# Performance work log

Hardware: AMD Instinct MI355X
Metric: run time of the kernel (lower is better)

The kernel has to match this reference:

```python
import jax, jax.numpy as jnp
import numpy as np

B, LINS, LHIS, LACT = 128, 64, 128, 32
VOCAB, ACTSZ = 2000, 100
INS_H, INS_E = 256, 128
ACT_E, ACT_IN, ACT_H = 128, 512, 512
POS_E, COL_E, COL_H = 32, 32, 32
ENV = 7 * (POS_E + COL_H)  # 448


def _lstm_cell(h, c, x, Wih, Whh, bih, bhh):
    # torch LSTM gate order: i, f, g, o
    g = x @ Wih.T + h @ Whh.T + bih + bhh
    i, f, gg, o = jnp.split(g, 4, axis=-1)
    c = jax.nn.sigmoid(f) * c + jax.nn.sigmoid(i) * jnp.tanh(gg)
    h = jax.nn.sigmoid(o) * jnp.tanh(c)
    return h, c


def _run_lstm(xs, Wih, Whh, bih, bhh):
    # xs: [T, N, D] -> hs: [T, N, H], zero initial state (torch default)
    N = xs.shape[1]
    H = Whh.shape[1]
    h0 = jnp.zeros((N, H), xs.dtype)

    def step(carry, x):
        h, c = carry
        h, c = _lstm_cell(h, c, x, Wih, Whh, bih, bhh)
        return (h, c), h

    _, hs = jax.lax.scan(step, (h0, h0), xs)
    return hs


def _bilstm_encode(tokens, emb, Wf, Uf, bf1, bf2, Wb, Ub, bb1, bb2):
    xs = emb[tokens].transpose(1, 0, 2)            # [L, B, E]
    hf = _run_lstm(xs, Wf, Uf, bf1, bf2)           # [L, B, H]
    hb = _run_lstm(xs[::-1], Wb, Ub, bb1, bb2)[::-1]
    return jnp.concatenate([hf, hb], -1).transpose(1, 0, 2)  # [B, L, 2H]


def _env_encode(tokens, color_emb, pos_emb, Wih, Whh, bih, bhh):
    # tokens: [B, 35] = 7 beakers x (id + 4 color slots)
    t = tokens.reshape(B, 7, 5)
    col = color_emb[t[:, :, 1:5]]                  # [B, 7, 4, COL_E]
    xs = col.reshape(B * 7, 4, COL_E).transpose(1, 0, 2)  # [4, B*7, COL_E]
    h_last = _run_lstm(xs, Wih, Whh, bih, bhh)[-1].reshape(B, 7, COL_H)
    pos = jnp.broadcast_to(pos_emb[None], (B, 7, POS_E))
    return jnp.concatenate([pos, h_last], -1).reshape(B, 7 * (POS_E + COL_H))


def _attend(A, H, q):
    # Faithful to attend(): scores = sum_k (H @ W)[b,l,k] * q[b,k]; softmax over l;
    # A = H @ W is query-independent so it is hoisted out of the decode loop.
    a = jax.nn.softmax(jnp.einsum('blk,bk->bl', A, q), axis=1)
    return jnp.einsum('bl,bld->bd', a, H)


def _forward(ins_tokens, his_tokens, actions, cur_env, ini_env,
             enc_emb, enc_Wih_f, enc_Whh_f, enc_bih_f, enc_bhh_f,
             enc_Wih_b, enc_Whh_b, enc_bih_b, enc_bhh_b,
             color_emb, pos_emb, ws_Wih, ws_Whh, ws_bih, ws_bhh,
             act_emb, W_c, W_p, W_sb1, W_sb2, W_sc1, W_sc2,
             Wbd_W, Wbd_b, dec_Wih, dec_Whh, dec_bih, dec_bhh,
             h2a_W, h2a_b, h0, c0):
    ins_enc = _bilstm_encode(ins_tokens, enc_emb, enc_Wih_f, enc_Whh_f, enc_bih_f,
                             enc_bhh_f, enc_Wih_b, enc_Whh_b, enc_bih_b, enc_bhh_b)
    his_enc = _bilstm_encode(his_tokens, enc_emb, enc_Wih_f, enc_Whh_f, enc_bih_f,
                             enc_bhh_f, enc_Wih_b, enc_Whh_b, enc_bih_b, enc_bhh_b)
    cur_ctx = _env_encode(cur_env, color_emb, pos_emb, ws_Wih, ws_Whh, ws_bih, ws_bhh)
    ini_ctx = _env_encode(ini_env, color_emb, pos_emb, ws_Wih, ws_Whh, ws_bih, ws_bhh)

    X = act_emb[actions]                            # [B, T, ACT_E]
    # Query-independent projections, hoisted out of the per-step loop (same math).
    A_c = jnp.einsum('bld,dk->blk', ins_enc, W_c)   # [B, LINS, ACT_H]
    A_p = jnp.einsum('bld,dk->blk', his_enc, W_p)   # [B, LHIS, ACT_H+2*INS_H]
    K = ACT_H + 2 * INS_H
    ini_rep = jnp.broadcast_to(ini_ctx[:, None, :], (B, LACT, ENV))
    cur_rep = jnp.broadcast_to(cur_ctx[:, None, :], (B, LACT, ENV))
    A_b1 = jnp.broadcast_to((ini_ctx @ W_sb1)[:, None, :], (B, LACT, K))
    A_b2 = jnp.broadcast_to((ini_ctx @ W_sb2)[:, None, :], (B, LACT, K))
    A_c1 = jnp.broadcast_to((cur_ctx @ W_sc1)[:, None, :], (B, LACT, K))
    A_c2 = jnp.broadcast_to((cur_ctx @ W_sc2)[:, None, :], (B, LACT, K))

    def step(carry, x_t):
        h, c = carry
        z_c = _attend(A_c, ins_enc, h)              # [B, 2*INS_H]
        q = jnp.concatenate([h, z_c], -1)           # [B, ACT_H+2*INS_H]
        z_p = _attend(A_p, his_enc, q)
        z_s1 = jnp.concatenate([_attend(A_b1, ini_rep, q),
                                _attend(A_b2, ini_rep, q)], -1)
        z_sk = jnp.concatenate([_attend(A_c1, cur_rep, q),
                                _attend(A_c2, cur_rep, q)], -1)
        hk1 = jnp.concatenate([z_c, z_p, z_s1, z_sk, x_t], -1)  # [B, 2944]
        hk = jnp.tanh(hk1 @ Wbd_W.T + Wbd_b)        # [B, ACT_IN]
        h, c = _lstm_cell(h, c, hk, dec_Wih, dec_Whh, dec_bih, dec_bhh)
        return (h, c), h

    _, outs = jax.lax.scan(step, (h0, c0), X.transpose(1, 0, 2))
    logits = outs.transpose(1, 0, 2) @ h2a_W.T + h2a_b  # [B, LACT, ACTSZ]
    return logits


def setup_inputs() -> dict:
    root = jax.random.key(0)
    ki = iter(jax.random.split(root, 40))

    def nrm(shape, s=0.05):
        return jax.random.normal(next(ki), shape, dtype=jnp.float32) * s

    inp = {}
    inp['ins_tokens'] = jax.random.randint(next(ki), (B, LINS), 0, VOCAB)
    inp['his_tokens'] = jax.random.randint(next(ki), (B, LHIS), 0, VOCAB)
    inp['actions'] = jax.random.randint(next(ki), (B, LACT), 0, ACTSZ)
    inp['cur_env'] = jax.random.randint(next(ki), (B, 35), 0, 7)
    inp['ini_env'] = jax.random.randint(next(ki), (B, 35), 0, 7)
    inp['enc_emb'] = nrm((VOCAB, INS_E))
    inp['enc_Wih_f'] = nrm((4 * INS_H, INS_E))
    inp['enc_Whh_f'] = nrm((4 * INS_H, INS_H))
    inp['enc_bih_f'] = nrm((4 * INS_H,))
    inp['enc_bhh_f'] = nrm((4 * INS_H,))
    inp['enc_Wih_b'] = nrm((4 * INS_H, INS_E))
    inp['enc_Whh_b'] = nrm((4 * INS_H, INS_H))
    inp['enc_bih_b'] = nrm((4 * INS_H,))
    inp['enc_bhh_b'] = nrm((4 * INS_H,))
    inp['color_emb'] = nrm((7, COL_E))
    inp['pos_emb'] = nrm((7, POS_E))
    inp['ws_Wih'] = nrm((4 * COL_H, COL_E))
    inp['ws_Whh'] = nrm((4 * COL_H, COL_H))
    inp['ws_bih'] = nrm((4 * COL_H,))
    inp['ws_bhh'] = nrm((4 * COL_H,))
    inp['act_emb'] = nrm((ACTSZ, ACT_E))
    inp['W_c'] = nrm((2 * INS_H, ACT_H))
    inp['W_p'] = nrm((2 * INS_H, 2 * INS_H + ACT_H))
    inp['W_sb1'] = nrm((ENV, ACT_H + 2 * INS_H))
    inp['W_sb2'] = nrm((ENV, ACT_H + 2 * INS_H))
    inp['W_sc1'] = nrm((ENV, ACT_H + 2 * INS_H))
    inp['W_sc2'] = nrm((ENV, ACT_H + 2 * INS_H))
    inp['Wbd_W'] = nrm((ACT_IN, 4 * ENV + 4 * INS_H + ACT_E))
    inp['Wbd_b'] = nrm((ACT_IN,))
    inp['dec_Wih'] = nrm((4 * ACT_H, ACT_IN))
    inp['dec_Whh'] = nrm((4 * ACT_H, ACT_H))
    inp['dec_bih'] = nrm((4 * ACT_H,))
    inp['dec_bhh'] = nrm((4 * ACT_H,))
    inp['h2a_W'] = nrm((ACTSZ, ACT_H))
    inp['h2a_b'] = nrm((ACTSZ,))
    inp['h0'] = nrm((B, ACT_H))
    inp['c0'] = nrm((B, ACT_H))
    return inp


def reference(ins_tokens, his_tokens, actions, cur_env, ini_env,
              enc_emb, enc_Wih_f, enc_Whh_f, enc_bih_f, enc_bhh_f,
              enc_Wih_b, enc_Whh_b, enc_bih_b, enc_bhh_b,
              color_emb, pos_emb, ws_Wih, ws_Whh, ws_bih, ws_bhh,
              act_emb, W_c, W_p, W_sb1, W_sb2, W_sc1, W_sc2,
              Wbd_W, Wbd_b, dec_Wih, dec_Whh, dec_bih, dec_bhh,
              h2a_W, h2a_b, h0, c0):
    return _forward(ins_tokens, his_tokens, actions, cur_env, ini_env,
                    enc_emb, enc_Wih_f, enc_Whh_f, enc_bih_f, enc_bhh_f,
                    enc_Wih_b, enc_Whh_b, enc_bih_b, enc_bhh_b,
                    color_emb, pos_emb, ws_Wih, ws_Whh, ws_bih, ws_bhh,
                    act_emb, W_c, W_p, W_sb1, W_sb2, W_sc1, W_sc2,
                    Wbd_W, Wbd_b, dec_Wih, dec_Whh, dec_bih, dec_bhh,
                    h2a_W, h2a_b, h0, c0)
```

## Files before the change

kernel.cpp:

```cpp
#include <hip/hip_runtime.h>


typedef unsigned short u16;
typedef __attribute__((ext_vector_type(8))) short bf16x8;
typedef __attribute__((ext_vector_type(4))) float f32x4;

#define DEVFN static __device__ __forceinline__

DEVFN float bf2f(u16 u) {
  unsigned int x = ((unsigned int)u) << 16;
  float f; __builtin_memcpy(&f, &x, 4); return f;
}
DEVFN u16 f2bf(float f) {
  unsigned int x; __builtin_memcpy(&x, &f, 4);
  x = (x + 0x7fffu + ((x >> 16) & 1u)) >> 16;
  return (u16)x;
}
DEVFN float sigf(float x) { return 1.f / (1.f + __expf(-x)); }
DEVFN bf16x8 load8(const u16* p) { return *(const bf16x8*)p; }
DEVFN int clampi(int v, int lo, int hi) { return v < lo ? lo : (v > hi ? hi : v); }

struct GemmArgs {
  const u16* A; int lda; int M;
  const u16* W; int ldw; int N; int K;
  void* out; int ldc;
  const float* bias;
  const float* hk_base; const float* proj_act; const int* actions; int t;
};

template <int EPI>
__global__ __launch_bounds__(256) void gemm_k(GemmArgs g) {
  int lane = threadIdx.x & 63;
  int wave = threadIdx.x >> 6;
  int col = lane & 15, q = lane >> 4;
  int m0 = blockIdx.x * 64 + (wave >> 1) * 32;
  int n0 = blockIdx.y * 64 + (wave & 1) * 32;
  f32x4 acc[2][2] = {};
  int rA[2] = { m0 + col, m0 + 16 + col };
  int rB[2] = { n0 + col, n0 + 16 + col };
  bool gA[2] = { rA[0] < g.M, rA[1] < g.M };
  bool gB[2] = { rB[0] < g.N, rB[1] < g.N };
  const u16* pA[2]; const u16* pB[2];
#pragma unroll
  for (int i = 0; i < 2; i++) {
    pA[i] = g.A + (size_t)(gA[i] ? rA[i] : 0) * g.lda + q * 8;
    pB[i] = g.W + (size_t)(gB[i] ? rB[i] : 0) * g.ldw + q * 8;
  }
  bf16x8 zf = {0,0,0,0,0,0,0,0};
  for (int k = 0; k < g.K; k += 32) {
    bf16x8 a0 = gA[0] ? load8(pA[0] + k) : zf;
    bf16x8 a1 = gA[1] ? load8(pA[1] + k) : zf;
    bf16x8 b0 = gB[0] ? load8(pB[0] + k) : zf;
    bf16x8 b1 = gB[1] ? load8(pB[1] + k) : zf;
    acc[0][0] = __builtin_amdgcn_mfma_f32_16x16x32_bf16(a0, b0, acc[0][0], 0, 0, 0);
    acc[0][1] = __builtin_amdgcn_mfma_f32_16x16x32_bf16(a0, b1, acc[0][1], 0, 0, 0);
    acc[1][0] = __builtin_amdgcn_mfma_f32_16x16x32_bf16(a1, b0, acc[1][0], 0, 0, 0);
    acc[1][1] = __builtin_amdgcn_mfma_f32_16x16x32_bf16(a1, b1, acc[1][1], 0, 0, 0);
  }
#pragma unroll
  for (int mi = 0; mi < 2; mi++)
#pragma unroll
    for (int ni = 0; ni < 2; ni++)
#pragma unroll
      for (int r = 0; r < 4; r++) {
        int m = m0 + mi * 16 + q * 4 + r;
        int n = n0 + ni * 16 + col;
        if (m >= g.M || n >= g.N) continue;
        float v = acc[mi][ni][r];
        if constexpr (EPI == 0) {
          if (g.bias) v += g.bias[n];
          ((float*)g.out)[(size_t)m * g.ldc + n] = v;
        } else {
          ((u16*)g.out)[(size_t)m * g.ldc + n] = f2bf(v);
        }
      }
}

template <int EPI>
__global__ __launch_bounds__(256) void gemm32_k(GemmArgs g) {
  int lane = threadIdx.x & 63;
  int wave = threadIdx.x >> 6;
  int col = lane & 15, q = lane >> 4;
  int m0 = blockIdx.x * 32 + (wave >> 1) * 16;
  int n0 = blockIdx.y * 32 + (wave & 1) * 16;
  f32x4 acc = {};
  int rA = m0 + col, rB = n0 + col;
  bool gA = rA < g.M, gB = rB < g.N;
  const u16* pA = g.A + (size_t)(gA ? rA : 0) * g.lda + q * 8;
  const u16* pB = g.W + (size_t)(gB ? rB : 0) * g.ldw + q * 8;
  bf16x8 zf = {0,0,0,0,0,0,0,0};
  for (int k = 0; k < g.K; k += 32) {
    bf16x8 a = gA ? load8(pA + k) : zf;
    bf16x8 b = gB ? load8(pB + k) : zf;
    acc = __builtin_amdgcn_mfma_f32_16x16x32_bf16(a, b, acc, 0, 0, 0);
  }
#pragma unroll
  for (int r = 0; r < 4; r++) {
    int m = m0 + q * 4 + r;
    int n = n0 + col;
    if (m >= g.M || n >= g.N) continue;
    float v = acc[r];
    if constexpr (EPI == 0) {
      if (g.bias) v += g.bias[n];
      ((float*)g.out)[(size_t)m * g.ldc + n] = v;
    } else {
      int act = clampi(g.actions[m * 32 + g.t], 0, 99);
      v += g.hk_base[m * 512 + n] + g.proj_act[(size_t)act * 512 + n];
      ((u16*)g.out)[(size_t)m * g.ldc + n] = f2bf(tanhf(v));
    }
  }
}

__global__ __launch_bounds__(256) void dec_gates_cell32(
    const u16* zin_cur, const u16* Wih, const u16* Whh, const float* bias_int,
    float* c_ws, u16* zin_nxt, u16* qbuf, u16* outs, int t) {
  int lane = threadIdx.x & 63, wave = threadIdx.x >> 6;
  int col = lane & 15, q = lane >> 4;
  int m0 = blockIdx.x * 32 + (wave >> 1) * 16;
  int n0 = blockIdx.y * 32 + (wave & 1) * 16;
  f32x4 acc = {};
  const u16* pA = zin_cur + (size_t)(m0 + col) * 1024 + q * 8;
  int r = n0 + col;
  int src = (r & 3) * 512 + (r >> 2);
  const u16* pI = Wih + (size_t)src * 512 + q * 8;
  const u16* pH = Whh + (size_t)src * 512 + q * 8;
  for (int k = 0; k < 512; k += 32) {
    acc = __builtin_amdgcn_mfma_f32_16x16x32_bf16(load8(pA + k), load8(pI + k), acc, 0, 0, 0);
  }
  for (int k = 0; k < 512; k += 32) {
    acc = __builtin_amdgcn_mfma_f32_16x16x32_bf16(load8(pA + 512 + k), load8(pH + k), acc, 0, 0, 0);
  }
  __shared__ float ls[32][36];
#pragma unroll
  for (int rr = 0; rr < 4; rr++) {
    int ml = (wave >> 1) * 16 + q * 4 + rr;
    int nl = (wave & 1) * 16 + col;
    ls[ml][nl] = acc[rr] + bias_int[blockIdx.y * 32 + nl];
  }
  __syncthreads();
  int m = threadIdx.x & 31, jloc = threadIdx.x >> 5;
  int gm = blockIdx.x * 32 + m;
  int j = blockIdx.y * 8 + jloc;
  float gi = ls[m][jloc * 4 + 0];
  float gf = ls[m][jloc * 4 + 1];
  float gg = ls[m][jloc * 4 + 2];
  float go = ls[m][jloc * 4 + 3];
  float cn = sigf(gf) * c_ws[gm * 512 + j] + sigf(gi) * tanhf(gg);
  c_ws[gm * 512 + j] = cn;
  float hn = sigf(go) * tanhf(cn);
  u16 hb = f2bf(hn);
  zin_nxt[(size_t)gm * 1024 + 512 + j] = hb;
  qbuf[(size_t)gm * 1024 + j] = hb;
  outs[((size_t)gm * 32 + t) * 512 + j] = hb;
}

struct CvtJob { const float* src; u16* dst; int R; int C; int ld; int c0; int tr; int blk0; };
struct CvtJobs { CvtJob j[15]; int njobs; };

__global__ void cvt_all(CvtJobs a) {
  int bid = blockIdx.x;
  int ji = 0;
  while (ji + 1 < a.njobs && bid >= a.j[ji + 1].blk0) ji++;
  CvtJob jb = a.j[ji];
  int idx = (bid - jb.blk0) * 256 + threadIdx.x;
  int n = jb.R * jb.C;
  if (idx >= n) return;
  int r = idx / jb.C, c = idx - r * jb.C;
  float v = jb.src[(size_t)r * jb.ld + jb.c0 + c];
  if (jb.tr) jb.dst[(size_t)c * jb.R + r] = f2bf(v);
  else jb.dst[idx] = f2bf(v);
}

__global__ void prep_small(
    const float* bih_f, const float* bhh_f, float* bias_f,
    const float* bih_b, const float* bhh_b, float* bias_b,
    const float* Wbd_b, float* bwbd,
    const float* h2a_b, float* bh2a,
    const float* dec_bih, const float* dec_bhh, float* bdecint) {
  int i = blockIdx.x * 256 + threadIdx.x;
  if (i < 1024) bias_f[i] = bih_f[i] + bhh_f[i];
  else if (i < 2048) { int k = i - 1024; bias_b[k] = bih_b[k] + bhh_b[k]; }
  else if (i < 2560) { int k = i - 2048; bwbd[k] = Wbd_b[k]; }
  else if (i < 2660) { int k = i - 2560; bh2a[k] = h2a_b[k]; }
  else if (i < 4708) {
    int r = i - 2660;
    int j = r >> 2, gg = r & 3;
    bdecint[r] = dec_bih[gg * 512 + j] + dec_bhh[gg * 512 + j];
  }
}

__global__ void wsum_build(const float* Wbd, u16* Wsum) {
  int idx = blockIdx.x * 256 + threadIdx.x;
  int n = idx / 896, j = idx % 896;
  int c1 = (j < 448) ? (1024 + j) : (1920 + (j - 448));
  int c2 = c1 + 448;
  Wsum[idx] = f2bf(Wbd[(size_t)n * 2944 + c1] + Wbd[(size_t)n * 2944 + c2]);
}

__global__ __launch_bounds__(256) void env_encode(
    const int* cur_env, const int* ini_env,
    const float* color_emb, const float* pos_emb,
    const float* wih, const float* whh, const float* bih, const float* bhh,
    u16* ctx_cat) {
  __shared__ float s_wih[128 * 33], s_whh[128 * 33], s_b[128], s_col[7 * 32];
  __shared__ float h_lds[8][33];
  int tid = threadIdx.x;
  for (int i = tid; i < 128 * 32; i += 256) {
    int r = i >> 5, k2 = i & 31;
    s_wih[r * 33 + k2] = wih[i];
    s_whh[r * 33 + k2] = whh[i];
  }
  for (int i = tid; i < 128; i += 256) s_b[i] = bih[i] + bhh[i];
  for (int i = tid; i < 224; i += 256) s_col[i] = color_emb[i];
  int sl = tid >> 5, j = tid & 31;
  int gseq = blockIdx.x * 8 + sl;
  int e = gseq / 896, rem = gseq % 896;
  int b = rem / 7, p = rem % 7;
  const int* env = e ? ini_env : cur_env;
  int eoff = e ? 0 : 448;
  h_lds[sl][j] = 0.f;
  __syncthreads();
  float cj = 0.f, hj = 0.f;
  for (int st = 0; st < 4; st++) {
    int tok = clampi(env[b * 35 + p * 5 + 1 + st], 0, 6);
    const float* x = &s_col[tok * 32];
    float pi = s_b[j], pf = s_b[32 + j], pg = s_b[64 + j], po = s_b[96 + j];
    for (int k = 0; k < 32; k++) {
      float xk = x[k], hk = h_lds[sl][k];
      pi += s_wih[j * 33 + k] * xk + s_whh[j * 33 + k] * hk;
      pf += s_wih[(32 + j) * 33 + k] * xk + s_whh[(32 + j) * 33 + k] * hk;
      pg += s_wih[(64 + j) * 33 + k] * xk + s_whh[(64 + j) * 33 + k] * hk;
      po += s_wih[(96 + j) * 33 + k] * xk + s_whh[(96 + j) * 33 + k] * hk;
    }
    cj = sigf(pf) * cj + sigf(pi) * tanhf(pg);
    hj = sigf(po) * tanhf(cj);
    __syncthreads();
    h_lds[sl][j] = hj;
    __syncthreads();
  }
  size_t base = (size_t)b * 896 + eoff + p * 64;
  ctx_cat[base + j] = f2bf(pos_emb[p * 32 + j]);
  ctx_cat[base + 32 + j] = f2bf(hj);
}

#define HBUF ((size_t)4 * 128 * 256)
__global__ __launch_bounds__(128) void enc_step3(
    int t, int chainbase,
    const int* ins_tok, const int* his_tok,
    const float* projE_f, const float* projE_b,
    const u16* whh_f, const u16* whh_b,
    const float* bias_f, const float* bias_b,
    u16* h_enc, float* c_enc,
    u16* ins_enc, u16* his_enc) {
  int chain = chainbase + (blockIdx.x >> 6);
  int sub = blockIdx.x & 63;
  int sgrp = sub >> 3, jq = sub & 7;
  int w = threadIdx.x >> 6, lane = threadIdx.x & 63;
  int col = lane & 15, q = lane >> 4;
  int dir = chain & 1, his = chain >> 1;
  int L = his ? 128 : 64;
  const int* toks = his ? his_tok : ins_tok;
  int t_x = dir ? (L - 1 - t) : t;
  const float* projE = dir ? projE_b : projE_f;
  const u16* whh = dir ? whh_b : whh_f;
  const float* bias = dir ? bias_b : bias_f;
  const u16* h_rd = h_enc + ((size_t)((t & 1) ^ 1)) * HBUF + (size_t)chain * 128 * 256;
  u16* h_wr = h_enc + ((size_t)(t & 1)) * HBUF + (size_t)chain * 128 * 256;
  float* c_g = c_enc + (size_t)chain * 128 * 256;
  u16* out = his ? his_enc : ins_enc;

  int jw = jq * 32 + w * 16;
  f32x4 acc[4] = {};
  if (t > 0) {
    const u16* hrow = h_rd + (size_t)(sgrp * 16 + col) * 256 + q * 8;
    const u16* wrow[4];
#pragma unroll
    for (int G = 0; G < 4; G++) wrow[G] = whh + (size_t)(G * 256 + jw + col) * 256 + q * 8;
    for (int k = 0; k < 256; k += 32) {
      bf16x8 a = load8(hrow + k);
#pragma unroll
      for (int G = 0; G < 4; G++) {
        bf16x8 bb = load8(wrow[G] + k);
        acc[G] = __builtin_amdgcn_mfma_f32_16x16x32_bf16(a, bb, acc[G], 0, 0, 0);
      }
    }
  }
  int j = jw + col;
  float bi = bias[j], bf = bias[256 + j], bg = bias[512 + j], bo = bias[768 + j];
#pragma unroll
  for (int r = 0; r < 4; r++) {
    int s = q * 4 + r;
    int b = sgrp * 16 + s;
    int tok = clampi(toks[b * L + t_x], 0, 1999);
    const float* px = projE + (size_t)tok * 1024;
    float pi = acc[0][r] + px[j] + bi;
    float pf = acc[1][r] + px[256 + j] + bf;
    float pg = acc[2][r] + px[512 + j] + bg;
    float po = acc[3][r] + px[768 + j] + bo;
    float cold = (t > 0) ? c_g[b * 256 + j] : 0.f;
    float cn = sigf(pf) * cold + sigf(pi) * tanhf(pg);
    float hn = sigf(po) * tanhf(cn);
    c_g[b * 256 + j] = cn;
    u16 hb = f2bf(hn);
    h_wr[b * 256 + j] = hb;
    out[((size_t)b * L + t_x) * 512 + dir * 256 + j] = hb;
  }
}

__global__ __launch_bounds__(256) void attn1(
    const u16* A_c, const u16* insenc, u16* qattn, u16* qbuf) {
  int b = blockIdx.x, tid = threadIdx.x;
  __shared__ float su[512], red[256], aw[64];
  __shared__ float zacc[4][512];
  for (int d = tid; d < 512; d += 256) su[d] = bf2f(qbuf[(size_t)b * 1024 + d]);
  __syncthreads();
  {
    int l = tid >> 2, part = tid & 3;
    const u16* row = A_c + ((size_t)b * 64 + l) * 512 + part * 128;
    float s = 0.f;
    for (int k = 0; k < 128; k += 8) {
      bf16x8 v = load8(row + k);
#pragma unroll
      for (int e = 0; e < 8; e++) s += bf2f((u16)v[e]) * su[part * 128 + k + e];
    }
    red[tid] = s;
  }
  __syncthreads();
  if (tid < 64) {
    float sc = red[tid * 4] + red[tid * 4 + 1] + red[tid * 4 + 2] + red[tid * 4 + 3];
    float m = sc;
    for (int off = 32; off > 0; off >>= 1) m = fmaxf(m, __shfl_xor(m, off));
    float e = __expf(sc - m);
    float sm = e;
    for (int off = 32; off > 0; off >>= 1) sm += __shfl_xor(sm, off);
    aw[tid] = e / sm;
  }
  __syncthreads();
  {
    int part = tid >> 6, chunk = tid & 63;
    float a[8] = {};
    for (int l = part * 16; l < part * 16 + 16; l++) {
      bf16x8 v = load8(insenc + ((size_t)b * 64 + l) * 512 + chunk * 8);
      float w = aw[l];
#pragma unroll
      for (int e = 0; e < 8; e++) a[e] += w * bf2f((u16)v[e]);
    }
#pragma unroll
    for (int e = 0; e < 8; e++) zacc[part][chunk * 8 + e] = a[e];
  }
  __syncthreads();
  for (int d = tid; d < 512; d += 256) {
    float z = zacc[0][d] + zacc[1][d] + zacc[2][d] + zacc[3][d];
    u16 zb = f2bf(z);
    qattn[(size_t)b * 1024 + d] = zb;
    qbuf[(size_t)b * 1024 + 512 + d] = zb;
  }
}

__global__ __launch_bounds__(256) void attn2(
    const float* u_p, const u16* hisenc, u16* qattn) {
  int b = blockIdx.x, tid = threadIdx.x;
  __shared__ float su[512], red[256], aw[128], mr[2];
  __shared__ float zacc[4][512];
  for (int d = tid; d < 512; d += 256) su[d] = u_p[b * 512 + d];
  __syncthreads();
  {
    int l = tid >> 1, part = tid & 1;
    const u16* row = hisenc + ((size_t)b * 128 + l) * 512 + part * 256;
    float s = 0.f;
    for (int k = 0; k < 256; k += 8) {
      bf16x8 v = load8(row + k);
#pragma unroll
      for (int e = 0; e < 8; e++) s += bf2f((u16)v[e]) * su[part * 256 + k + e];
    }
    red[tid] = s;
  }
  __syncthreads();
  float sc = (tid < 128) ? red[tid * 2] + red[tid * 2 + 1] : 0.f;
  __syncthreads();
  if (tid < 128) red[tid] = sc;
  __syncthreads();
  if (tid < 64) {
    float m = fmaxf(red[tid], red[tid + 64]);
    for (int off = 32; off > 0; off >>= 1) m = fmaxf(m, __shfl_xor(m, off));
    if (tid == 0) mr[0] = m;
  }
  __syncthreads();
  float ex = 0.f;
  if (tid < 128) { ex = __expf(sc - mr[0]); red[tid] = ex; }
  __syncthreads();
  if (tid < 64) {
    float s2 = red[tid] + red[tid + 64];
    for (int off = 32; off > 0; off >>= 1) s2 += __shfl_xor(s2, off);
    if (tid == 0) mr[1] = s2;
  }
  __syncthreads();
  if (tid < 128) aw[tid] = ex / mr[1];
  __syncthreads();
  {
    int part = tid >> 6, chunk = tid & 63;
    float a[8] = {};
    for (int l = part * 32; l < part * 32 + 32; l++) {
      bf16x8 v = load8(hisenc + ((size_t)b * 128 + l) * 512 + chunk * 8);
      float w = aw[l];
#pragma unroll
      for (int e = 0; e < 8; e++) a[e] += w * bf2f((u16)v[e]);
    }
#pragma unroll
    for (int e = 0; e < 8; e++) zacc[part][chunk * 8 + e] = a[e];
  }
  __syncthreads();
  for (int d = tid; d < 512; d += 256) {
    float z = zacc[0][d] + zacc[1][d] + zacc[2][d] + zacc[3][d];
    qattn[(size_t)b * 1024 + 512 + d] = f2bf(z);
  }
}

__global__ void dec_init(const float* h0, const float* c0, u16* zin0, u16* qbuf, float* c_ws) {
  int idx = blockIdx.x * 256 + threadIdx.x;
  int b = idx >> 9, d = idx & 511;
  u16 hv = f2bf(h0[idx]);
  zin0[(size_t)b * 1024 + 512 + d] = hv;
  qbuf[(size_t)b * 1024 + d] = hv;
  c_ws[idx] = c0[idx];
}

extern "C" void kernel_launch(void* const* d_in, const int* in_sizes, int n_in,
                              void* d_out, int out_size, void* d_ws, size_t ws_size,
                              hipStream_t stream) {
  const int* ins_tok = (const int*)d_in[0];
  const int* his_tok = (const int*)d_in[1];
  const int* actions = (const int*)d_in[2];
  const int* cur_env = (const int*)d_in[3];
  const int* ini_env = (const int*)d_in[4];
  const float* enc_emb = (const float*)d_in[5];
  const float* Wih_f = (const float*)d_in[6];
  const float* Whh_f = (const float*)d_in[7];
  const float* bih_f = (const float*)d_in[8];
  const float* bhh_f = (const float*)d_in[9];
  const float* Wih_b = (const float*)d_in[10];
  const float* Whh_b = (const float*)d_in[11];
  const float* bih_b = (const float*)d_in[12];
  const float* bhh_b = (const float*)d_in[13];
  const float* color_emb = (const float*)d_in[14];
  const float* pos_emb = (const float*)d_in[15];
  const float* ws_Wih = (const float*)d_in[16];
  const float* ws_Whh = (const float*)d_in[17];
  const float* ws_bih = (const float*)d_in[18];
  const float* ws_bhh = (const float*)d_in[19];
  const float* act_emb = (const float*)d_in[20];
  const float* W_c = (const float*)d_in[21];
  const float* W_p = (const float*)d_in[22];
  const float* Wbd_W = (const float*)d_in[27];
  const float* Wbd_b = (const float*)d_in[28];
  const float* dec_Wih = (const float*)d_in[29];
  const float* dec_Whh = (const float*)d_in[30];
  const float* dec_bih = (const float*)d_in[31];
  const float* dec_bhh = (const float*)d_in[32];
  const float* h2a_W = (const float*)d_in[33];
  const float* h2a_b = (const float*)d_in[34];
  const float* h0 = (const float*)d_in[35];
  const float* c0 = (const float*)d_in[36];
  (void)in_sizes; (void)n_in; (void)out_size; (void)ws_size;

  char* ws = (char*)d_ws;
  size_t off = 0;
  auto alloc = [&](size_t bytes) -> char* {
    char* p = ws + off;
    off = (off + bytes + 255) & ~(size_t)255;
    return p;
  };
  u16* insenc   = (u16*)alloc(8192ull * 512 * 2);
  u16* hisenc   = (u16*)alloc(16384ull * 512 * 2);
  u16* outs     = (u16*)alloc(4096ull * 512 * 2);
  u16* Wsum     = (u16*)alloc(512ull * 896 * 2);
  u16* h_enc    = (u16*)alloc(2 * HBUF * 2);
  float* c_enc  = (float*)alloc(4ull * 128 * 256 * 4);
  float* projact= (float*)alloc(100ull * 512 * 4);
  float* bias_f = (float*)alloc(1024 * 4);
  float* bias_b = (float*)alloc(1024 * 4);
  float* bdecint= (float*)alloc(2048 * 4);
  float* bwbd   = (float*)alloc(512 * 4);
  float* bh2a   = (float*)alloc(128 * 4);
  u16* ctxcat   = (u16*)alloc(128ull * 896 * 2);
  float* hkbase = (float*)alloc(128ull * 512 * 4);
  float* u_p    = (float*)alloc(128ull * 512 * 4);
  u16* qbuf     = (u16*)alloc(128ull * 1024 * 2);
  u16* qattn    = (u16*)alloc(128ull * 1024 * 2);
  u16* zin      = (u16*)alloc(2ull * 128 * 1024 * 2);
  float* c_dec  = (float*)alloc(128ull * 512 * 4);
  float* projE_f = (float*)alloc(2000ull * 1024 * 4);
  float* projE_b = (float*)alloc(2000ull * 1024 * 4);
  u16* A_c      = (u16*)alloc(8192ull * 512 * 2);
  u16* emb_bf   = (u16*)alloc(2000ull * 128 * 2);
  u16* wihf_bf  = (u16*)alloc(1024ull * 128 * 2);
  u16* wihb_bf  = (u16*)alloc(1024ull * 128 * 2);
  u16* whhf_bf  = (u16*)alloc(1024ull * 256 * 2);
  u16* whhb_bf  = (u16*)alloc(1024ull * 256 * 2);
  u16* act_bf   = (u16*)alloc(100ull * 128 * 2);
  u16* wcT_bf   = (u16*)alloc(512ull * 512 * 2);
  u16* wp_bf    = (u16*)alloc(512ull * 1024 * 2);
  u16* wbd01_bf = (u16*)alloc(512ull * 1024 * 2);
  u16* wbdx_bf  = (u16*)alloc(512ull * 128 * 2);
  u16* dwih_bf  = (u16*)alloc(2048ull * 512 * 2);
  u16* dwhh_bf  = (u16*)alloc(2048ull * 512 * 2);
  u16* h2a_bf   = (u16*)alloc(100ull * 512 * 2);

  CvtJobs cj{};
  int nb = 0, jn = 0;
  auto addjob = [&](const float* s, u16* d, int R, int C, int ld, int c0c, int tr) {
    cj.j[jn] = { s, d, R, C, ld, c0c, tr, nb };
    nb += (R * C + 255) / 256;
    jn++;
  };
  addjob(enc_emb, emb_bf, 2000, 128, 128, 0, 0);
  addjob(Wih_f, wihf_bf, 1024, 128, 128, 0, 0);
  addjob(Wih_b, wihb_bf, 1024, 128, 128, 0, 0);
  addjob(Whh_f, whhf_bf, 1024, 256, 256, 0, 0);
  addjob(Whh_b, whhb_bf, 1024, 256, 256, 0, 0);
  addjob(act_emb, act_bf, 100, 128, 128, 0, 0);
  addjob(W_c, wcT_bf, 512, 512, 512, 0, 1);
  addjob(W_p, wp_bf, 512, 1024, 1024, 0, 0);
  addjob(Wbd_W, wbd01_bf, 512, 1024, 2944, 0, 0);
  addjob(Wbd_W, wbdx_bf, 512, 128, 2944, 2816, 0);
  addjob(dec_Wih, dwih_bf, 2048, 512, 512, 0, 0);
  addjob(dec_Whh, dwhh_bf, 2048, 512, 512, 0, 0);
  addjob(h2a_W, h2a_bf, 100, 512, 512, 0, 0);
  cj.njobs = jn;
  cvt_all<<<nb, 256, 0, stream>>>(cj);

  prep_small<<<19, 256, 0, stream>>>(bih_f, bhh_f, bias_f, bih_b, bhh_b, bias_b,
                                     Wbd_b, bwbd, h2a_b, bh2a,
                                     dec_bih, dec_bhh, bdecint);
  wsum_build<<<1792, 256, 0, stream>>>(Wbd_W, Wsum);

  {
    GemmArgs ge = {};
    ge.A = emb_bf; ge.lda = 128; ge.M = 2000; ge.W = wihf_bf; ge.ldw = 128;
    ge.N = 1024; ge.K = 128; ge.out = projE_f; ge.ldc = 1024;
    gemm_k<0><<<dim3(32, 16), 256, 0, stream>>>(ge);
    ge.W = wihb_bf; ge.out = projE_b;
    gemm_k<0><<<dim3(32, 16), 256, 0, stream>>>(ge);
  }

  GemmArgs gp = {};
  gp.A = act_bf; gp.lda = 128; gp.M = 100; gp.W = wbdx_bf; gp.ldw = 128;
  gp.N = 512; gp.K = 128; gp.out = projact; gp.ldc = 512; gp.bias = bwbd;
  gemm_k<0><<<dim3(2, 8), 256, 0, stream>>>(gp);

  env_encode<<<224, 256, 0, stream>>>(cur_env, ini_env, color_emb, pos_emb,
                                      ws_Wih, ws_Whh, ws_bih, ws_bhh, ctxcat);
  GemmArgs gb = {};
  gb.A = ctxcat; gb.lda = 896; gb.M = 128; gb.W = Wsum; gb.ldw = 896;
  gb.N = 512; gb.K = 896; gb.out = hkbase; gb.ldc = 512;
  gemm_k<0><<<dim3(2, 8), 256, 0, stream>>>(gb);

  for (int t = 0; t < 128; t++) {
    int cb = (t < 64) ? 0 : 2;
    int nbk = (t < 64) ? 256 : 128;
    enc_step3<<<nbk, 128, 0, stream>>>(t, cb, ins_tok, his_tok,
                                       projE_f, projE_b, whhf_bf, whhb_bf,
                                       bias_f, bias_b, h_enc, c_enc,
                                       insenc, hisenc);
  }

  {
    GemmArgs ga = {};
    ga.A = insenc; ga.lda = 512; ga.M = 8192; ga.W = wcT_bf; ga.ldw = 512;
    ga.N = 512; ga.K = 512; ga.out = A_c; ga.ldc = 512;
    gemm_k<1><<<dim3(128, 8), 256, 0, stream>>>(ga);
  }

  dec_init<<<256, 256, 0, stream>>>(h0, c0, zin, qbuf, c_dec);
  for (int t = 0; t < 32; t++) {
    u16* zin_cur = zin + (size_t)(t & 1) * 128 * 1024;
    u16* zin_nxt = zin + (size_t)((t + 1) & 1) * 128 * 1024;
    attn1<<<128, 256, 0, stream>>>(A_c, insenc, qattn, qbuf);
    GemmArgs gv = {};
    gv.A = qbuf; gv.lda = 1024; gv.M = 128; gv.W = wp_bf; gv.ldw = 1024;
    gv.N = 512; gv.K = 1024; gv.out = u_p; gv.ldc = 512;
    gemm32_k<0><<<dim3(4, 16), 256, 0, stream>>>(gv);
    attn2<<<128, 256, 0, stream>>>(u_p, hisenc, qattn);
    GemmArgs gh = {};
    gh.A = qattn; gh.lda = 1024; gh.M = 128; gh.W = wbd01_bf; gh.ldw = 1024;
    gh.N = 512; gh.K = 1024; gh.out = zin_cur; gh.ldc = 1024;
    gh.hk_base = hkbase; gh.proj_act = projact; gh.actions = actions; gh.t = t;
    gemm32_k<2><<<dim3(4, 16), 256, 0, stream>>>(gh);
    dec_gates_cell32<<<dim3(4, 64), 256, 0, stream>>>(
        zin_cur, dwih_bf, dwhh_bf, bdecint, c_dec, zin_nxt, qbuf, outs, t);
  }

  GemmArgs gl = {};
  gl.A = outs; gl.lda = 512; gl.M = 4096; gl.W = h2a_bf; gl.ldw = 512;
  gl.N = 100; gl.K = 512; gl.out = d_out; gl.ldc = 100; gl.bias = bh2a;
  gemm32_k<0><<<dim3(128, 4), 256, 0, stream>>>(gl);
}
```

Measured before the change: 2.716 ms.

## Widen decoder attention blocks, split u_p GEMM over K halves, fold dec_init into prep

Both attention kernels in the decode loop now use 512 threads per block, so each thread covers half as much of the score and context reductions. The W_p projection GEMM is split into two K-halves that write separate partial outputs, doubling the grid; attn2 adds the two partials when it loads its query. The decoder state initialisation moves into prep_small to save one launch. The aim is more parallelism and shorter per-step latency in the 32-step decode loop, at the cost of more shared memory per block and an extra partial buffer.

```diff
diff --git a/kernel.cpp b/kernel.cpp
--- a/kernel.cpp
+++ b/kernel.cpp
@@ -111,6 +111,30 @@
   }
 }
 
+__global__ __launch_bounds__(256) void up_split(
+    const u16* qbuf, const u16* wp, float* u_p2) {
+  int lane = threadIdx.x & 63;
+  int wave = threadIdx.x >> 6;
+  int col = lane & 15, q = lane >> 4;
+  int half = blockIdx.y >> 4;
+  int by = blockIdx.y & 15;
+  int m0 = blockIdx.x * 32 + (wave >> 1) * 16;
+  int n0 = by * 32 + (wave & 1) * 16;
+  f32x4 acc = {};
+  const u16* pA = qbuf + (size_t)(m0 + col) * 1024 + half * 512 + q * 8;
+  const u16* pB = wp + (size_t)(n0 + col) * 1024 + half * 512 + q * 8;
+  for (int k = 0; k < 512; k += 32) {
+    acc = __builtin_amdgcn_mfma_f32_16x16x32_bf16(load8(pA + k), load8(pB + k), acc, 0, 0, 0);
+  }
+  float* out = u_p2 + (size_t)half * 128 * 512;
+#pragma unroll
+  for (int r = 0; r < 4; r++) {
+    int m = m0 + q * 4 + r;
+    int n = n0 + col;
+    out[(size_t)m * 512 + n] = acc[r];
+  }
+}
+
 __global__ __launch_bounds__(256) void dec_gates_cell32(
     const u16* zin_cur, const u16* Wih, const u16* Whh, const float* bias_int,
     float* c_ws, u16* zin_nxt, u16* qbuf, u16* outs, int t) {
@@ -176,7 +200,8 @@
     const float* bih_b, const float* bhh_b, float* bias_b,
     const float* Wbd_b, float* bwbd,
     const float* h2a_b, float* bh2a,
-    const float* dec_bih, const float* dec_bhh, float* bdecint) {
+    const float* dec_bih, const float* dec_bhh, float* bdecint,
+    const float* h0, const float* c0, u16* zin0, u16* qbuf, float* c_ws) {
   int i = blockIdx.x * 256 + threadIdx.x;
   if (i < 1024) bias_f[i] = bih_f[i] + bhh_f[i];
   else if (i < 2048) { int k = i - 1024; bias_b[k] = bih_b[k] + bhh_b[k]; }
@@ -186,6 +211,13 @@
     int r = i - 2660;
     int j = r >> 2, gg = r & 3;
     bdecint[r] = dec_bih[gg * 512 + j] + dec_bhh[gg * 512 + j];
+  } else if (i < 4708 + 128 * 512) {
+    int k = i - 4708;
+    int b = k >> 9, d = k & 511;
+    u16 hv = f2bf(h0[k]);
+    zin0[(size_t)b * 1024 + 512 + d] = hv;
+    qbuf[(size_t)b * 1024 + d] = hv;
+    c_ws[k] = c0[k];
   }
 }
 
@@ -307,27 +339,29 @@
   }
 }
 
-__global__ __launch_bounds__(256) void attn1(
+__global__ __launch_bounds__(512) void attn1(
     const u16* A_c, const u16* insenc, u16* qattn, u16* qbuf) {
   int b = blockIdx.x, tid = threadIdx.x;
-  __shared__ float su[512], red[256], aw[64];
-  __shared__ float zacc[4][512];
-  for (int d = tid; d < 512; d += 256) su[d] = bf2f(qbuf[(size_t)b * 1024 + d]);
-  __syncthreads();
-  {
-    int l = tid >> 2, part = tid & 3;
-    const u16* row = A_c + ((size_t)b * 64 + l) * 512 + part * 128;
+  __shared__ float su[512], red[512], aw[64];
+  __shared__ float zacc[8][512];
+  su[tid] = bf2f(qbuf[(size_t)b * 1024 + tid]);
+  __syncthreads();
+  {
+    int l = tid >> 3, part = tid & 7;
+    const u16* row = A_c + ((size_t)b * 64 + l) * 512 + part * 64;
     float s = 0.f;
-    for (int k = 0; k < 128; k += 8) {
+    for (int k = 0; k < 64; k += 8) {
       bf16x8 v = load8(row + k);
 #pragma unroll
-      for (int e = 0; e < 8; e++) s += bf2f((u16)v[e]) * su[part * 128 + k + e];
+      for (int e = 0; e < 8; e++) s += bf2f((u16)v[e]) * su[part * 64 + k + e];
     }
     red[tid] = s;
   }
   __syncthreads();
   if (tid < 64) {
-    float sc = red[tid * 4] + red[tid * 4 + 1] + red[tid * 4 + 2] + red[tid * 4 + 3];
+    float sc = 0.f;
+#pragma unroll
+    for (int i = 0; i < 8; i++) sc += red[tid * 8 + i];
     float m = sc;
     for (int off = 32; off > 0; off >>= 1) m = fmaxf(m, __shfl_xor(m, off));
     float e = __expf(sc - m);
@@ -339,7 +373,7 @@
   {
     int part = tid >> 6, chunk = tid & 63;
     float a[8] = {};
-    for (int l = part * 16; l < part * 16 + 16; l++) {
+    for (int l = part * 8; l < part * 8 + 8; l++) {
       bf16x8 v = load8(insenc + ((size_t)b * 64 + l) * 512 + chunk * 8);
       float w = aw[l];
 #pragma unroll
@@ -349,34 +383,36 @@
     for (int e = 0; e < 8; e++) zacc[part][chunk * 8 + e] = a[e];
   }
   __syncthreads();
-  for (int d = tid; d < 512; d += 256) {
-    float z = zacc[0][d] + zacc[1][d] + zacc[2][d] + zacc[3][d];
+  {
+    float z = zacc[0][tid] + zacc[1][tid] + zacc[2][tid] + zacc[3][tid]
+            + zacc[4][tid] + zacc[5][tid] + zacc[6][tid] + zacc[7][tid];
     u16 zb = f2bf(z);
-    qattn[(size_t)b * 1024 + d] = zb;
-    qbuf[(size_t)b * 1024 + 512 + d] = zb;
-  }
-}
-
-__global__ __launch_bounds__(256) void attn2(
-    const float* u_p, const u16* hisenc, u16* qattn) {
+    qattn[(size_t)b * 1024 + tid] = zb;
+    qbuf[(size_t)b * 1024 + 512 + tid] = zb;
+  }
+}
+
+__global__ __launch_bounds__(512) void attn2(
+    const float* u_p2, const u16* hisenc, u16* qattn) {
   int b = blockIdx.x, tid = threadIdx.x;
-  __shared__ float su[512], red[256], aw[128], mr[2];
-  __shared__ float zacc[4][512];
-  for (int d = tid; d < 512; d += 256) su[d] = u_p[b * 512 + d];
-  __syncthreads();
-  {
-    int l = tid >> 1, part = tid & 1;
-    const u16* row = hisenc + ((size_t)b * 128 + l) * 512 + part * 256;
+  __shared__ float su[512], red[512], aw[128], mr[2];
+  __shared__ float zacc[8][512];
+  su[tid] = u_p2[(size_t)b * 512 + tid] + u_p2[65536 + (size_t)b * 512 + tid];
+  __syncthreads();
+  {
+    int l = tid >> 2, part = tid & 3;
+    const u16* row = hisenc + ((size_t)b * 128 + l) * 512 + part * 128;
     float s = 0.f;
-    for (int k = 0; k < 256; k += 8) {
+    for (int k = 0; k < 128; k += 8) {
       bf16x8 v = load8(row + k);
 #pragma unroll
-      for (int e = 0; e < 8; e++) s += bf2f((u16)v[e]) * su[part * 256 + k + e];
+      for (int e = 0; e < 8; e++) s += bf2f((u16)v[e]) * su[part * 128 + k + e];
     }
     red[tid] = s;
   }
   __syncthreads();
-  float sc = (tid < 128) ? red[tid * 2] + red[tid * 2 + 1] : 0.f;
+  float sc = 0.f;
+  if (tid < 128) sc = red[tid * 4] + red[tid * 4 + 1] + red[tid * 4 + 2] + red[tid * 4 + 3];
   __syncthreads();
   if (tid < 128) red[tid] = sc;
   __syncthreads();
@@ -400,7 +436,7 @@
   {
     int part = tid >> 6, chunk = tid & 63;
     float a[8] = {};
-    for (int l = part * 32; l < part * 32 + 32; l++) {
+    for (int l = part * 16; l < part * 16 + 16; l++) {
       bf16x8 v = load8(hisenc + ((size_t)b * 128 + l) * 512 + chunk * 8);
       float w = aw[l];
 #pragma unroll
@@ -410,19 +446,11 @@
     for (int e = 0; e < 8; e++) zacc[part][chunk * 8 + e] = a[e];
   }
   __syncthreads();
-  for (int d = tid; d < 512; d += 256) {
-    float z = zacc[0][d] + zacc[1][d] + zacc[2][d] + zacc[3][d];
-    qattn[(size_t)b * 1024 + 512 + d] = f2bf(z);
-  }
-}
-
-__global__ void dec_init(const float* h0, const float* c0, u16* zin0, u16* qbuf, float* c_ws) {
-  int idx = blockIdx.x * 256 + threadIdx.x;
-  int b = idx >> 9, d = idx & 511;
-  u16 hv = f2bf(h0[idx]);
-  zin0[(size_t)b * 1024 + 512 + d] = hv;
-  qbuf[(size_t)b * 1024 + d] = hv;
-  c_ws[idx] = c0[idx];
+  {
+    float z = zacc[0][tid] + zacc[1][tid] + zacc[2][tid] + zacc[3][tid]
+            + zacc[4][tid] + zacc[5][tid] + zacc[6][tid] + zacc[7][tid];
+    qattn[(size_t)b * 1024 + 512 + tid] = f2bf(z);
+  }
 }
 
 extern "C" void kernel_launch(void* const* d_in, const int* in_sizes, int n_in,
@@ -484,7 +512,7 @@
   float* bh2a   = (float*)alloc(128 * 4);
   u16* ctxcat   = (u16*)alloc(128ull * 896 * 2);
   float* hkbase = (float*)alloc(128ull * 512 * 4);
-  float* u_p    = (float*)alloc(128ull * 512 * 4);
+  float* u_p2   = (float*)alloc(2ull * 128 * 512 * 4);
   u16* qbuf     = (u16*)alloc(128ull * 1024 * 2);
   u16* qattn    = (u16*)alloc(128ull * 1024 * 2);
   u16* zin      = (u16*)alloc(2ull * 128 * 1024 * 2);
@@ -529,9 +557,10 @@
   cj.njobs = jn;
   cvt_all<<<nb, 256, 0, stream>>>(cj);
 
-  prep_small<<<19, 256, 0, stream>>>(bih_f, bhh_f, bias_f, bih_b, bhh_b, bias_b,
-                                     Wbd_b, bwbd, h2a_b, bh2a,
-                                     dec_bih, dec_bhh, bdecint);
+  prep_small<<<(4708 + 128 * 512 + 255) / 256, 256, 0, stream>>>(
+      bih_f, bhh_f, bias_f, bih_b, bhh_b, bias_b,
+      Wbd_b, bwbd, h2a_b, bh2a, dec_bih, dec_bhh, bdecint,
+      h0, c0, zin, qbuf, c_dec);
   wsum_build<<<1792, 256, 0, stream>>>(Wbd_W, Wsum);
 
   {
@@ -571,16 +600,12 @@
     gemm_k<1><<<dim3(128, 8), 256, 0, stream>>>(ga);
   }
 
-  dec_init<<<256, 256, 0, stream>>>(h0, c0, zin, qbuf, c_dec);
   for (int t = 0; t < 32; t++) {
     u16* zin_cur = zin + (size_t)(t & 1) * 128 * 1024;
     u16* zin_nxt = zin + (size_t)((t + 1) & 1) * 128 * 1024;
-    attn1<<<128, 256, 0, stream>>>(A_c, insenc, qattn, qbuf);
-    GemmArgs gv = {};
-    gv.A = qbuf; gv.lda = 1024; gv.M = 128; gv.W = wp_bf; gv.ldw = 1024;
-    gv.N = 512; gv.K = 1024; gv.out = u_p; gv.ldc = 512;
-    gemm32_k<0><<<dim3(4, 16), 256, 0, stream>>>(gv);
-    attn2<<<128, 256, 0, stream>>>(u_p, hisenc, qattn);
+    attn1<<<128, 512, 0, stream>>>(A_c, insenc, qattn, qbuf);
+    up_split<<<dim3(4, 32), 256, 0, stream>>>(qbuf, wp_bf, u_p2);
+    attn2<<<128, 512, 0, stream>>>(u_p2, hisenc, qattn);
     GemmArgs gh = {};
     gh.A = qattn; gh.lda = 1024; gh.M = 128; gh.W = wbd01_bf; gh.ldw = 1024;
     gh.N = 512; gh.K = 1024; gh.out = zin_cur; gh.ldc = 1024;
```

Measured after the change: 2.531 ms, median of 2. -6.8%, faster.
